# Kernel optimization log

Hardware: AMD Instinct MI355X
Metric: run time of the kernel (lower is better)

## Reference

```python
import jax, jax.numpy as jnp
import numpy as np

B, Tu, Tm, Tz = 32, 128, 128, 32
V, H, E = 10000, 512, 128
S = E + H  # state_size


def setup_inputs() -> dict:
    key = jax.random.key(0)
    ks = jax.random.split(key, 24)
    u_input = jax.random.randint(ks[0], (B, Tu), 0, V)
    m_input = jax.random.randint(ks[1], (B, Tm), 0, V)
    pv_z_idx = jax.random.randint(ks[2], (B, Tz), 0, V)
    inp = {
        'u_input': u_input,
        'u_input_1hot': jax.nn.one_hot(u_input, V, dtype=jnp.float32),
        'u_hiddens': jax.random.normal(ks[3], (B, Tu, H), jnp.float32),
        'm_input': m_input,
        'm_input_1hot': jax.nn.one_hot(m_input, V, dtype=jnp.float32),
        'm_hiddens': jax.random.normal(ks[4], (B, Tm, H), jnp.float32),
        'pv_z_prob': jax.nn.softmax(jax.random.normal(ks[5], (B, Tz, V), jnp.float32), axis=-1),
        'pv_z_hidden': jax.random.normal(ks[6], (B, Tz, H), jnp.float32),
        'pv_z_idx': pv_z_idx,
        'emb_zt': jax.random.normal(ks[7], (B, 1, E), jnp.float32),
        'last_hidden': jax.random.normal(ks[8], (1, B, H), jnp.float32),
        # Attn params (concat attention: v . tanh(W [h; enc]))
        'W_attn': jax.random.normal(ks[9], (H, 2 * H), jnp.float32) * 0.02,
        'b_attn': jnp.zeros((H,), jnp.float32),
        'v_attn': jax.random.normal(ks[10], (H,), jnp.float32) * 0.05,
        # GRU params (torch gate order r,z,n)
        'W_ih': jax.random.normal(ks[11], (3 * H, S), jnp.float32) * 0.02,
        'W_hh': jax.random.normal(ks[12], (3 * H, H), jnp.float32) * 0.02,
        'b_ih': jnp.zeros((3 * H,), jnp.float32),
        'b_hh': jnp.zeros((3 * H,), jnp.float32),
        # generation / copy-score projections
        'W_gen': jax.random.normal(ks[13], (V, S), jnp.float32) * 0.02,
        'b_gen': jnp.zeros((V,), jnp.float32),
        'W_cpu': jax.random.normal(ks[14], (S, H), jnp.float32) * 0.02,
        'b_cpu': jnp.zeros((S,), jnp.float32),
        'W_cpm': jax.random.normal(ks[15], (S, H), jnp.float32) * 0.02,
        'b_cpm': jnp.zeros((S,), jnp.float32),
        'W_cppz': jax.random.normal(ks[16], (S, H), jnp.float32) * 0.02,
        'b_cppz': jnp.zeros((S,), jnp.float32),
    }
    return inp


def reference(u_input, u_input_1hot, u_hiddens, m_input, m_input_1hot, m_hiddens,
              pv_z_prob, pv_z_hidden, pv_z_idx, emb_zt, last_hidden,
              W_attn, b_attn, v_attn, W_ih, W_hh, b_ih, b_hh,
              W_gen, b_gen, W_cpu, b_cpu, W_cpm, b_cpm, W_cppz, b_cppz):
    Bv, Tuv, Vv = u_input_1hot.shape
    Tmv = m_hiddens.shape[1]
    t_input = emb_zt  # [B,1,E] (enable_selc_read=False)

    # ---- concat attention over [u; m; pv_z] hiddens ----
    enc = jnp.concatenate([u_hiddens, m_hiddens, pv_z_hidden], axis=1)  # [B,T,H]
    h0 = jnp.transpose(last_hidden, (1, 0, 2))  # [B,1,H]
    hid_rep = jnp.broadcast_to(h0, (Bv, enc.shape[1], h0.shape[2]))
    energy = jnp.tanh(jnp.einsum('bth,gh->btg', jnp.concatenate([hid_rep, enc], axis=2), W_attn) + b_attn)
    attn_w = jax.nn.softmax(jnp.einsum('bth,h->bt', energy, v_attn), axis=1)
    context = jnp.einsum('bt,bth->bh', attn_w, enc)[:, None, :]  # [B,1,H]

    # ---- single GRU step (torch gate order r,z,n) ----
    x = jnp.concatenate([t_input, context], axis=2)[:, 0, :]  # [B,E+H]
    h = h0[:, 0, :]
    gi = x @ W_ih.T + b_ih
    gh = h @ W_hh.T + b_hh
    i_r, i_z, i_n = jnp.split(gi, 3, axis=1)
    h_r, h_z, h_n = jnp.split(gh, 3, axis=1)
    r = jax.nn.sigmoid(i_r + h_r)
    z = jax.nn.sigmoid(i_z + h_z)
    n = jnp.tanh(i_n + r * h_n)
    h_new = (1.0 - z) * n + z * h  # [B,H]
    gru_out = h_new[:, None, :]
    last_hidden_new = h_new[None, :, :]

    # ---- generation + copy scores ----
    st = jnp.concatenate([h_new, t_input[:, 0, :]], axis=1)  # [B,E+H]
    score_g = st @ W_gen.T + b_gen  # [B,V]
    sc_u = jnp.einsum('bts,bs->bt', jnp.tanh(jnp.einsum('bth,sh->bts', u_hiddens, W_cpu) + b_cpu), st)
    sc_m = jnp.einsum('bts,bs->bt', jnp.tanh(jnp.einsum('bth,sh->bts', m_hiddens, W_cpm) + b_cpm), st)
    sc_pz = jnp.einsum('bts,bs->bt', jnp.tanh(jnp.einsum('bth,sh->bts', pv_z_hidden, W_cppz) + b_cppz), st)
    probs = jax.nn.softmax(jnp.concatenate([score_g, sc_u, sc_m, sc_pz], axis=1), axis=1)

    p_g = probs[:, :Vv]
    p_u = probs[:, Vv:Vv + Tuv]
    p_m = probs[:, Vv + Tuv:Vv + Tuv + Tmv]
    p_pz = probs[:, Vv + Tuv + Tmv:]
    prob_out = (p_g
                + jnp.einsum('bt,btv->bv', p_u, u_input_1hot)
                + jnp.einsum('bt,btv->bv', p_m, m_input_1hot)
                + jnp.einsum('bt,btv->bv', p_pz, pv_z_prob))
    return (prob_out, last_hidden_new, gru_out)
```

## Files before the change

### kernel.cpp

```cpp
#include <hip/hip_runtime.h>
#include <math.h>

#define B   32
#define TU  128
#define TM  128
#define TZ  32
#define TENC 288
#define V   10000
#define H   512
#define E   128
#define S   640
#define G3  1536
#define NLOG (V + TENC)

#define WS_Q      0
#define WS_SCORE  (WS_Q + B*H)
#define WS_CTX    (WS_SCORE + B*TENC)
#define WS_GI     (WS_CTX + B*H)
#define WS_GH     (WS_GI + B*G3)
#define WS_ST     (WS_GH + B*G3)
#define WS_LOGIT  (WS_ST + B*S)
#define WS_PCOPY  (WS_LOGIT + B*NLOG)
#define WS_F_TOTAL (WS_PCOPY + B*TENC)

#define BF_WA2  0
#define BF_WCP  (BF_WA2 + 512*512)
#define BF_ENC  (BF_WCP + 3*640*512)
#define BF_ST   (BF_ENC + B*TENC*H)
#define BF_TANH (BF_ST + B*S)

typedef __attribute__((ext_vector_type(8))) short bf16x8_t;
typedef __attribute__((ext_vector_type(4))) float f32x4_t;
typedef __attribute__((ext_vector_type(16))) float f32x16_t;

__device__ __forceinline__ float fast_tanh(float x) {
    return 1.f - 2.f / (__expf(2.f * x) + 1.f);
}

__device__ __forceinline__ unsigned short f2bf(float x) {
    unsigned int u = __float_as_uint(x);
    u += 0x7fffu + ((u >> 16) & 1u);
    return (unsigned short)(u >> 16);
}

__device__ __forceinline__ float bf2f(unsigned short u) {
    return __uint_as_float(((unsigned int)u) << 16);
}

__device__ __forceinline__ bf16x8_t cvt8(const float* p) {
    float4 a = *(const float4*)(p);
    float4 b = *(const float4*)(p + 4);
    bf16x8_t r;
    r[0] = (short)f2bf(a.x); r[1] = (short)f2bf(a.y);
    r[2] = (short)f2bf(a.z); r[3] = (short)f2bf(a.w);
    r[4] = (short)f2bf(b.x); r[5] = (short)f2bf(b.y);
    r[6] = (short)f2bf(b.z); r[7] = (short)f2bf(b.w);
    return r;
}

__device__ __forceinline__ const float* enc_row(const float* u, const float* m,
                                                const float* pz, int b, int t) {
    if (t < TU) return u + ((size_t)b * TU + t) * H;
    if (t < TU + TM) return m + ((size_t)b * TM + (t - TU)) * H;
    return pz + ((size_t)b * TZ + (t - TU - TM)) * H;
}

#define CVT_WA2_END  65536
#define CVT_TOTAL    (CVT_WA2_END + 3*81920)
#define CVTE_TOTAL   (B * TENC * 128)
#define CVT_ALL      (CVT_TOTAL + CVTE_TOTAL)
#define NMV          112
__global__ __launch_bounds__(256) void k_prep(const float* __restrict__ W_attn,
                                              const float* __restrict__ W_cpu,
                                              const float* __restrict__ W_cpm,
                                              const float* __restrict__ W_cppz,
                                              const float* __restrict__ u_h,
                                              const float* __restrict__ m_h,
                                              const float* __restrict__ pz_h,
                                              const float* __restrict__ last_h,
                                              const float* __restrict__ emb,
                                              const float* __restrict__ W_hh,
                                              const float* __restrict__ W_ih,
                                              const float* __restrict__ b_attn,
                                              const float* __restrict__ b_hh,
                                              const float* __restrict__ b_ih,
                                              float* __restrict__ ws,
                                              unsigned short* __restrict__ bf) {
    int blk = blockIdx.x, tid = threadIdx.x;
    __shared__ float redmv[4][64][16];
    if (blk < NMV) {
        int wave = tid >> 6, lane = tid & 63;
        int m = lane & 31, khalf = lane >> 5;
        f32x16_t acc = {};
        int n;
        if (blk < 16) {
            n = blk * 32 + m;
            const float* aptr = last_h + (size_t)m * H + khalf * 8;
            const float* bptr = W_attn + (size_t)n * 1024 + khalf * 8;
            for (int k0 = wave * 128; k0 < wave * 128 + 128; k0 += 16)
                acc = __builtin_amdgcn_mfma_f32_32x32x16_bf16(cvt8(aptr + k0),
                                                              cvt8(bptr + k0), acc, 0, 0, 0);
        } else if (blk < 64) {
            n = (blk - 16) * 32 + m;
            const float* aptr = last_h + (size_t)m * H + khalf * 8;
            const float* bptr = W_hh + (size_t)n * H + khalf * 8;
            for (int k0 = wave * 128; k0 < wave * 128 + 128; k0 += 16)
                acc = __builtin_amdgcn_mfma_f32_32x32x16_bf16(cvt8(aptr + k0),
                                                              cvt8(bptr + k0), acc, 0, 0, 0);
        } else {
            n = (blk - 64) * 32 + m;
            const float* aptr = emb + (size_t)m * E + khalf * 8;
            const float* bptr = W_ih + (size_t)n * S + khalf * 8;
            for (int k0 = wave * 32; k0 < wave * 32 + 32; k0 += 16)
                acc = __builtin_amdgcn_mfma_f32_32x32x16_bf16(cvt8(aptr + k0),
                                                              cvt8(bptr + k0), acc, 0, 0, 0);
        }
#pragma unroll
        for (int r = 0; r < 16; ++r) redmv[wave][lane][r] = acc[r];
        __syncthreads();
        if (wave == 0) {
#pragma unroll
            for (int r = 0; r < 16; ++r) {
                float v = redmv[0][lane][r] + redmv[1][lane][r] +
                          redmv[2][lane][r] + redmv[3][lane][r];
                int row = (r & 3) + 8 * (r >> 2) + 4 * khalf;
                if (blk < 16)      ws[WS_Q  + row * H  + n] = v + b_attn[n];
                else if (blk < 64) ws[WS_GH + row * G3 + n] = v + b_hh[n];
                else               ws[WS_GI + row * G3 + n] = v + b_ih[n];
            }
        }
        return;
    }
    int idx = (blk - NMV) * 256 + tid;
    if (idx >= CVT_ALL) return;
    const float* src;
    unsigned short* dst;
    if (idx < CVT_WA2_END) {
        int g = idx >> 7, c4 = idx & 127;
        int k = c4 * 4, kt = k >> 5, kin = k & 31;
        src = W_attn + (size_t)g * 1024 + 512 + k;
        dst = bf + BF_WA2 + kt * (512 * 32) + g * 32 + kin;
    } else if (idx < CVT_TOTAL) {
        int r = idx - CVT_WA2_END;
        int seg = r / 81920, q = r % 81920;
        int s = q >> 7, c4 = q & 127;
        int k = c4 * 4, kt = k >> 5, kin = k & 31;
        const float* s0 = (seg == 0) ? W_cpu : (seg == 1) ? W_cpm : W_cppz;
        src = s0 + (size_t)s * 512 + k;
        dst = bf + BF_WCP + seg * 327680 + kt * (640 * 32) + s * 32 + kin;
    } else {
        int e = idx - CVT_TOTAL;
        int b = e / (TENC * 128);
        int r = e % (TENC * 128);
        int t = r >> 7, c4 = r & 127;
        int k = c4 * 4, kt = k >> 5, kin = k & 31;
        src = enc_row(u_h, m_h, pz_h, b, t) + k;
        dst = bf + BF_ENC + (((size_t)b * 16 + kt) * TENC + t) * 32 + kin;
    }
    float4 v = *(const float4*)src;
    ushort4 o;
    o.x = f2bf(v.x); o.y = f2bf(v.y); o.z = f2bf(v.z); o.w = f2bf(v.w);
    *(ushort4*)dst = o;
}

__global__ __launch_bounds__(256) void k_enc_mfma(const unsigned short* __restrict__ bf,
                                                  const float* __restrict__ v_attn,
                                                  const float* __restrict__ b_cpu,
                                                  const float* __restrict__ b_cpm,
                                                  const float* __restrict__ b_cppz,
                                                  float* __restrict__ ws,
                                                  unsigned short* __restrict__ bft) {
    int blk = blockIdx.x;
    int typeC = blk & 1;
    int idx = blk >> 1;
    int b = idx / 9, t0 = (idx % 9) * 32;
    int tid = threadIdx.x, wave = tid >> 6, lane = tid & 63;
    int n16 = lane & 15, quad = lane >> 4;
    const unsigned short* abase =
        bf + BF_ENC + (((size_t)b * 16) * TENC + t0 + n16) * 32 + quad * 8;
    if (!typeC) {
        const unsigned short* wa =
            bf + BF_WA2 + (wave * 8) * (16 * 32) + n16 * 32 + quad * 8;
        f32x4_t acc[2][8];
#pragma unroll
        for (int tl = 0; tl < 2; ++tl)
#pragma unroll
            for (int j = 0; j < 8; ++j) acc[tl][j] = (f32x4_t){0.f, 0.f, 0.f, 0.f};
        for (int kt = 0; kt < 16; ++kt) {
            bf16x8_t a0 = *(const bf16x8_t*)(abase + (size_t)kt * TENC * 32);
            bf16x8_t a1 = *(const bf16x8_t*)(abase + (size_t)kt * TENC * 32 + 16 * 32);
            const unsigned short* wak = wa + (size_t)kt * 512 * 32;
#pragma unroll
            for (int j = 0; j < 8; ++j) {
                bf16x8_t bb = *(const bf16x8_t*)(wak + j * (16 * 32));
                acc[0][j] = __builtin_amdgcn_mfma_f32_16x16x32_bf16(a0, bb, acc[0][j], 0, 0, 0);
                acc[1][j] = __builtin_amdgcn_mfma_f32_16x16x32_bf16(a1, bb, acc[1][j], 0, 0, 0);
            }
        }
        float sval[2][4] = {{0.f, 0.f, 0.f, 0.f}, {0.f, 0.f, 0.f, 0.f}};
#pragma unroll
        for (int j = 0; j < 8; ++j) {
            int g = (wave * 8 + j) * 16 + n16;
            float q = ws[WS_Q + b * H + g];
            float va = v_attn[g];
#pragma unroll
            for (int tl = 0; tl < 2; ++tl)
#pragma unroll
                for (int r = 0; r < 4; ++r)
                    sval[tl][r] += fast_tanh(acc[tl][j][r] + q) * va;
        }
#pragma unroll
        for (int tl = 0; tl < 2; ++tl)
#pragma unroll
            for (int r = 0; r < 4; ++r)
#pragma unroll
                for (int off = 8; off > 0; off >>= 1)
                    sval[tl][r] += __shfl_down(sval[tl][r], off, 64);
        __shared__ float red[4][32];
        if (n16 == 0)
#pragma unroll
            for (int tl = 0; tl < 2; ++tl)
#pragma unroll
                for (int r = 0; r < 4; ++r)
                    red[wave][tl * 16 + quad * 4 + r] = sval[tl][r];
        __syncthreads();
        if (tid < 32)
            ws[WS_SCORE + b * TENC + t0 + tid] =
                red[0][tid] + red[1][tid] + red[2][tid] + red[3][tid];
    } else {
        int seg = (t0 < TU) ? 0 : (t0 < TU + TM) ? 1 : 2;
        const float* bias = (seg == 0) ? b_cpu : (seg == 1) ? b_cpm : b_cppz;
        const unsigned short* wc =
            bf + BF_WCP + seg * 327680 + (wave * 10) * (16 * 32) + n16 * 32 + quad * 8;
        f32x4_t acc[2][10];
#pragma unroll
        for (int tl = 0; tl < 2; ++tl)
#pragma unroll
            for (int j = 0; j < 10; ++j) acc[tl][j] = (f32x4_t){0.f, 0.f, 0.f, 0.f};
        for (int kt = 0; kt < 16; ++kt) {
            bf16x8_t a0 = *(const bf16x8_t*)(abase + (size_t)kt * TENC * 32);
            bf16x8_t a1 = *(const bf16x8_t*)(abase + (size_t)kt * TENC * 32 + 16 * 32);
            const unsigned short* wck = wc + (size_t)kt * 640 * 32;
#pragma unroll
            for (int j = 0; j < 10; ++j) {
                bf16x8_t bb = *(const bf16x8_t*)(wck + j * (16 * 32));
                acc[0][j] = __builtin_amdgcn_mfma_f32_16x16x32_bf16(a0, bb, acc[0][j], 0, 0, 0);
                acc[1][j] = __builtin_amdgcn_mfma_f32_16x16x32_bf16(a1, bb, acc[1][j], 0, 0, 0);
            }
        }
#pragma unroll
        for (int j = 0; j < 10; ++j) {
            int s = (wave * 10 + j) * 16 + n16;
            float bi = bias[s];
#pragma unroll
            for (int tl = 0; tl < 2; ++tl)
#pragma unroll
                for (int r = 0; r < 4; ++r) {
                    int t = t0 + tl * 16 + quad * 4 + r;
                    bft[BF_TANH + ((size_t)b * TENC + t) * S + s] =
                        f2bf(fast_tanh(acc[tl][j][r] + bi));
                }
        }
    }
}

__global__ __launch_bounds__(256) void k_softmax_ctx(const unsigned short* __restrict__ bf,
                                                     float* __restrict__ ws) {
    int b = blockIdx.x, tid = threadIdx.x;
    __shared__ float wsm[TENC];
    __shared__ float red1[4], red2[4];
    float local = -1e30f;
    for (int t = tid; t < TENC; t += 256) {
        float s = ws[WS_SCORE + b * TENC + t];
        wsm[t] = s;
        local = fmaxf(local, s);
    }
    int lane = tid & 63, wv = tid >> 6;
    for (int off = 32; off > 0; off >>= 1) local = fmaxf(local, __shfl_down(local, off, 64));
    if (lane == 0) red1[wv] = local;
    __syncthreads();
    float mx = fmaxf(fmaxf(red1[0], red1[1]), fmaxf(red1[2], red1[3]));
    float ls = 0.f;
    for (int t = tid; t < TENC; t += 256) {
        float e = __expf(wsm[t] - mx);
        wsm[t] = e;
        ls += e;
    }
    for (int off = 32; off > 0; off >>= 1) ls += __shfl_down(ls, off, 64);
    if (lane == 0) red2[wv] = ls;
    __syncthreads();
    float inv = 1.f / (red2[0] + red2[1] + red2[2] + red2[3]);

    int h2 = tid * 2;
    int kt = h2 >> 5, hin = h2 & 31;
    const unsigned short* ep = bf + BF_ENC + ((size_t)b * 16 + kt) * TENC * 32 + hin;
    float a00 = 0.f, a01 = 0.f, a10 = 0.f, a11 = 0.f;
#pragma unroll 2
    for (int t = 0; t < TENC; t += 2) {
        ushort2 v0 = *(const ushort2*)(ep + (size_t)t * 32);
        ushort2 v1 = *(const ushort2*)(ep + (size_t)(t + 1) * 32);
        float w0 = wsm[t], w1 = wsm[t + 1];
        a00 += w0 * bf2f(v0.x); a10 += w0 * bf2f(v0.y);
        a01 += w1 * bf2f(v1.x); a11 += w1 * bf2f(v1.y);
    }
    ws[WS_CTX + b * H + h2]     = (a00 + a01) * inv;
    ws[WS_CTX + b * H + h2 + 1] = (a10 + a11) * inv;
}

__global__ __launch_bounds__(256) void k_gru_ctx(const float* __restrict__ W_ih,
                                                 float* __restrict__ ws) {
    int blk = blockIdx.x, tid = threadIdx.x;
    __shared__ float redmv[4][64][16];
    int wave = tid >> 6, lane = tid & 63;
    int m = lane & 31, khalf = lane >> 5;
    int n = blk * 32 + m;
    const float* aptr = ws + WS_CTX + (size_t)m * H + khalf * 8;
    const float* bptr = W_ih + (size_t)n * S + E + khalf * 8;
    f32x16_t acc = {};
    for (int k0 = wave * 128; k0 < wave * 128 + 128; k0 += 16)
        acc = __builtin_amdgcn_mfma_f32_32x32x16_bf16(cvt8(aptr + k0),
                                                      cvt8(bptr + k0), acc, 0, 0, 0);
#pragma unroll
    for (int r = 0; r < 16; ++r) redmv[wave][lane][r] = acc[r];
    __syncthreads();
    if (wave == 0) {
#pragma unroll
        for (int r = 0; r < 16; ++r) {
            float v = redmv[0][lane][r] + redmv[1][lane][r] +
                      redmv[2][lane][r] + redmv[3][lane][r];
            int row = (r & 3) + 8 * (r >> 2) + 4 * khalf;
            ws[WS_GI + row * G3 + n] += v;
        }
    }
}

__global__ __launch_bounds__(256) void k_combine(const float* __restrict__ emb,
                                                 const float* __restrict__ last_hidden,
                                                 float* __restrict__ ws,
                                                 unsigned short* __restrict__ bf,
                                                 float* __restrict__ out) {
    int i = blockIdx.x * 256 + threadIdx.x;
    int b = i >> 9, h = i & 511;
    float gi_r = ws[WS_GI + b * G3 + h];
    float gi_z = ws[WS_GI + b * G3 + H + h];
    float gi_n = ws[WS_GI + b * G3 + 2 * H + h];
    float gh_r = ws[WS_GH + b * G3 + h];
    float gh_z = ws[WS_GH + b * G3 + H + h];
    float gh_n = ws[WS_GH + b * G3 + 2 * H + h];
    float rr = 1.f / (1.f + __expf(-(gi_r + gh_r)));
    float zz = 1.f / (1.f + __expf(-(gi_z + gh_z)));
    float nn = fast_tanh(gi_n + rr * gh_n);
    float hp = last_hidden[b * H + h];
    float hn = (1.f - zz) * nn + zz * hp;
    out[V * B + b * H + h] = hn;
    out[V * B + B * H + b * H + h] = hn;
    ws[WS_ST + b * S + h] = hn;
    bf[BF_ST + b * S + h] = f2bf(hn);
    if (h < E) {
        float ev = emb[b * E + h];
        ws[WS_ST + b * S + H + h] = ev;
        bf[BF_ST + b * S + H + h] = f2bf(ev);
    }
}

__global__ __launch_bounds__(256) void k_logits(const unsigned short* __restrict__ bf,
                                                const float* __restrict__ W_gen,
                                                const float* __restrict__ b_gen,
                                                float* __restrict__ ws) {
    int blk = blockIdx.x, tid = threadIdx.x;
    __shared__ float shmem[4 * 64 * 16];
    int wave = tid >> 6, lane = tid & 63;
    if (blk < 576) {
        int b = blk / 18, t0 = (blk % 18) * 16;
        float* st_s = shmem;
        for (int i = tid; i < S; i += 256) st_s[i] = ws[WS_ST + b * S + i];
        __syncthreads();
#pragma unroll
        for (int tl = 0; tl < 4; ++tl) {
            int t = t0 + wave * 4 + tl;
            const unsigned short* row = bf + BF_TANH + ((size_t)b * TENC + t) * S;
            float acc = 0.f;
#pragma unroll
            for (int i = 0; i < 10; ++i) {
                int s = lane + 64 * i;
                acc += bf2f(row[s]) * st_s[s];
            }
            for (int off = 32; off > 0; off >>= 1) acc += __shfl_down(acc, off, 64);
            if (lane == 0) ws[WS_LOGIT + (size_t)b * NLOG + V + t] = acc;
        }
    } else {
        float (*redmv)[64][16] = (float (*)[64][16])shmem;
        int m = lane & 31, khalf = lane >> 5;
        int n = (blk - 576) * 32 + m;
        int nr = (n < V) ? n : (V - 1);
        const unsigned short* aptr = bf + BF_ST + (size_t)m * S + khalf * 8;
        const float* bptr = W_gen + (size_t)nr * S + khalf * 8;
        f32x16_t acc = {};
        for (int k0 = wave * 160; k0 < wave * 160 + 160; k0 += 16)
            acc = __builtin_amdgcn_mfma_f32_32x32x16_bf16(*(const bf16x8_t*)(aptr + k0),
                                                          cvt8(bptr + k0), acc, 0, 0, 0);
#pragma unroll
        for (int r = 0; r < 16; ++r) redmv[wave][lane][r] = acc[r];
        __syncthreads();
        if (wave == 0 && n < V) {
            float bg = b_gen[n];
#pragma unroll
            for (int r = 0; r < 16; ++r) {
                float v = redmv[0][lane][r] + redmv[1][lane][r] +
                          redmv[2][lane][r] + redmv[3][lane][r];
                int row = (r & 3) + 8 * (r >> 2) + 4 * khalf;
                ws[WS_LOGIT + (size_t)row * NLOG + n] = v + bg;
            }
        }
    }
}

__global__ __launch_bounds__(512) void k_softmax_scatter(const int* __restrict__ u_in,
                                                         const int* __restrict__ m_in,
                                                         float* __restrict__ ws,
                                                         float* __restrict__ out) {
    int b = blockIdx.x, tid = threadIdx.x;
    __shared__ float red1[8], red2[8];
    __shared__ float ex[NLOG];
    const float* lg = ws + WS_LOGIT + (size_t)b * NLOG;
    float mx = -1e30f;
    for (int i = tid; i < NLOG; i += 512) {
        float v = lg[i];
        ex[i] = v;
        mx = fmaxf(mx, v);
    }
    int lane = tid & 63, wv = tid >> 6;
    for (int off = 32; off > 0; off >>= 1) mx = fmaxf(mx, __shfl_down(mx, off, 64));
    if (lane == 0) red1[wv] = mx;
    __syncthreads();
    mx = red1[0];
#pragma unroll
    for (int w = 1; w < 8; ++w) mx = fmaxf(mx, red1[w]);
    float sm = 0.f;
    for (int i = tid; i < NLOG; i += 512) {
        float e = __expf(ex[i] - mx);
        ex[i] = e;
        sm += e;
    }
    for (int off = 32; off > 0; off >>= 1) sm += __shfl_down(sm, off, 64);
    if (lane == 0) red2[wv] = sm;
    __syncthreads();
    sm = red2[0];
#pragma unroll
    for (int w = 1; w < 8; ++w) sm += red2[w];
    float inv = 1.f / sm;
    for (int i = tid; i < V; i += 512) out[b * V + i] = ex[i] * inv;
    __syncthreads();
    if (tid < TU + TM) {
        int idx = (tid < TU) ? u_in[b * TU + tid] : m_in[b * TM + (tid - TU)];
        atomicAdd(&out[(size_t)b * V + idx], ex[V + tid] * inv);
    } else if (tid < TENC) {
        ws[WS_PCOPY + b * TENC + tid] = ex[V + tid] * inv;
    }
}

__global__ __launch_bounds__(256) void k_pv(const float* __restrict__ pvp,
                                            const float* __restrict__ ws,
                                            float* __restrict__ out) {
    int b = blockIdx.y;
    int v = blockIdx.x * 256 + threadIdx.x;
    __shared__ float p[TZ];
    if (threadIdx.x < TZ) p[threadIdx.x] = ws[WS_PCOPY + b * TENC + TU + TM + threadIdx.x];
    __syncthreads();
    if (v >= V) return;
    float acc = 0.f;
#pragma unroll 4
    for (int t = 0; t < TZ; ++t) acc += p[t] * pvp[((size_t)b * TZ + t) * V + v];
    out[(size_t)b * V + v] += acc;
}

extern "C" void kernel_launch(void* const* d_in, const int* in_sizes, int n_in,
                              void* d_out, int out_size, void* d_ws, size_t ws_size,
                              hipStream_t stream) {
    const int*   u_input   = (const int*)d_in[0];
    const float* u_h       = (const float*)d_in[2];
    const int*   m_input   = (const int*)d_in[3];
    const float* m_h       = (const float*)d_in[5];
    const float* pv_prob   = (const float*)d_in[6];
    const float* pz_h      = (const float*)d_in[7];
    const float* emb       = (const float*)d_in[9];
    const float* last_h    = (const float*)d_in[10];
    const float* W_attn    = (const float*)d_in[11];
    const float* b_attn    = (const float*)d_in[12];
    const float* v_attn    = (const float*)d_in[13];
    const float* W_ih      = (const float*)d_in[14];
    const float* W_hh      = (const float*)d_in[15];
    const float* b_ih      = (const float*)d_in[16];
    const float* b_hh      = (const float*)d_in[17];
    const float* W_gen     = (const float*)d_in[18];
    const float* b_gen     = (const float*)d_in[19];
    const float* W_cpu     = (const float*)d_in[20];
    const float* b_cpu     = (const float*)d_in[21];
    const float* W_cpm     = (const float*)d_in[22];
    const float* b_cpm     = (const float*)d_in[23];
    const float* W_cppz    = (const float*)d_in[24];
    const float* b_cppz    = (const float*)d_in[25];
    float* ws  = (float*)d_ws;
    unsigned short* bf = (unsigned short*)(ws + WS_F_TOTAL);
    float* out = (float*)d_out;

    hipLaunchKernelGGL(k_prep, dim3(NMV + CVT_ALL / 256), dim3(256), 0, stream,
                       W_attn, W_cpu, W_cpm, W_cppz, u_h, m_h, pz_h,
                       last_h, emb, W_hh, W_ih, b_attn, b_hh, b_ih, ws, bf);
    hipLaunchKernelGGL(k_enc_mfma, dim3(576), dim3(256), 0, stream,
                       bf, v_attn, b_cpu, b_cpm, b_cppz, ws, bf);
    hipLaunchKernelGGL(k_softmax_ctx, dim3(B), dim3(256), 0, stream, bf, ws);
    hipLaunchKernelGGL(k_gru_ctx, dim3(48), dim3(256), 0, stream, W_ih, ws);
    hipLaunchKernelGGL(k_combine, dim3(64), dim3(256), 0, stream, emb, last_h, ws, bf, out);
    hipLaunchKernelGGL(k_logits, dim3(576 + 313), dim3(256), 0, stream, bf, W_gen, b_gen, ws);
    hipLaunchKernelGGL(k_softmax_scatter, dim3(B), dim3(512), 0, stream,
                       u_input, m_input, ws, out);
    hipLaunchKernelGGL(k_pv, dim3(40, B), dim3(256), 0, stream, pv_prob, ws, out);
}
```

Measured before the change: 513.1 us.

## Stage encoder-MFMA weight and activation tiles through LDS per K-step

The encoder MFMA kernel now cooperatively copies each K-slice of the weight matrix and the 32-row activation tile into shared memory, with barriers around each step. Waves then read their MFMA fragments from LDS instead of issuing scattered global loads. Block assignment also changes from interleaving the two block types to running all attention-score blocks first and copy-score blocks after. This aims for coalesced global loads, but it adds two barriers per K-step, has no double buffering, and uses about 42KB of LDS per block, which may limit occupancy.

```diff
diff --git a/kernel.cpp b/kernel.cpp
--- a/kernel.cpp
+++ b/kernel.cpp
@@ -170,32 +170,46 @@
                                                   const float* __restrict__ b_cppz,
                                                   float* __restrict__ ws,
                                                   unsigned short* __restrict__ bft) {
+    __shared__ __attribute__((aligned(16))) unsigned short lds_w[640 * 32];
+    __shared__ __attribute__((aligned(16))) unsigned short lds_a[32 * 32];
+    __shared__ float red[4][32];
     int blk = blockIdx.x;
-    int typeC = blk & 1;
-    int idx = blk >> 1;
+    int typeC = (blk >= 288);
+    int idx = typeC ? blk - 288 : blk;
     int b = idx / 9, t0 = (idx % 9) * 32;
     int tid = threadIdx.x, wave = tid >> 6, lane = tid & 63;
     int n16 = lane & 15, quad = lane >> 4;
-    const unsigned short* abase =
-        bf + BF_ENC + (((size_t)b * 16) * TENC + t0 + n16) * 32 + quad * 8;
+    const unsigned short* asrc0 =
+        bf + BF_ENC + (((size_t)b * 16) * TENC + t0) * 32;
     if (!typeC) {
-        const unsigned short* wa =
-            bf + BF_WA2 + (wave * 8) * (16 * 32) + n16 * 32 + quad * 8;
         f32x4_t acc[2][8];
 #pragma unroll
         for (int tl = 0; tl < 2; ++tl)
 #pragma unroll
             for (int j = 0; j < 8; ++j) acc[tl][j] = (f32x4_t){0.f, 0.f, 0.f, 0.f};
         for (int kt = 0; kt < 16; ++kt) {
-            bf16x8_t a0 = *(const bf16x8_t*)(abase + (size_t)kt * TENC * 32);
-            bf16x8_t a1 = *(const bf16x8_t*)(abase + (size_t)kt * TENC * 32 + 16 * 32);
-            const unsigned short* wak = wa + (size_t)kt * 512 * 32;
+            const unsigned short* wsrc = bf + BF_WA2 + (size_t)kt * (512 * 32);
+#pragma unroll
+            for (int c = 0; c < 8; ++c) {
+                int u = (c * 256 + tid) * 8;
+                *(bf16x8_t*)&lds_w[u] = *(const bf16x8_t*)&wsrc[u];
+            }
+            if (tid < 128) {
+                int u = tid * 8;
+                *(bf16x8_t*)&lds_a[u] =
+                    *(const bf16x8_t*)&asrc0[(size_t)kt * TENC * 32 + u];
+            }
+            __syncthreads();
+            bf16x8_t a0 = *(const bf16x8_t*)&lds_a[n16 * 32 + quad * 8];
+            bf16x8_t a1 = *(const bf16x8_t*)&lds_a[(n16 + 16) * 32 + quad * 8];
 #pragma unroll
             for (int j = 0; j < 8; ++j) {
-                bf16x8_t bb = *(const bf16x8_t*)(wak + j * (16 * 32));
+                bf16x8_t bb = *(const bf16x8_t*)
+                    &lds_w[((wave * 8 + j) * 16 + n16) * 32 + quad * 8];
                 acc[0][j] = __builtin_amdgcn_mfma_f32_16x16x32_bf16(a0, bb, acc[0][j], 0, 0, 0);
                 acc[1][j] = __builtin_amdgcn_mfma_f32_16x16x32_bf16(a1, bb, acc[1][j], 0, 0, 0);
             }
+            __syncthreads();
         }
         float sval[2][4] = {{0.f, 0.f, 0.f, 0.f}, {0.f, 0.f, 0.f, 0.f}};
 #pragma unroll
@@ -216,7 +230,6 @@
 #pragma unroll
                 for (int off = 8; off > 0; off >>= 1)
                     sval[tl][r] += __shfl_down(sval[tl][r], off, 64);
-        __shared__ float red[4][32];
         if (n16 == 0)
 #pragma unroll
             for (int tl = 0; tl < 2; ++tl)
@@ -230,23 +243,35 @@
     } else {
         int seg = (t0 < TU) ? 0 : (t0 < TU + TM) ? 1 : 2;
         const float* bias = (seg == 0) ? b_cpu : (seg == 1) ? b_cpm : b_cppz;
-        const unsigned short* wc =
-            bf + BF_WCP + seg * 327680 + (wave * 10) * (16 * 32) + n16 * 32 + quad * 8;
         f32x4_t acc[2][10];
 #pragma unroll
         for (int tl = 0; tl < 2; ++tl)
 #pragma unroll
             for (int j = 0; j < 10; ++j) acc[tl][j] = (f32x4_t){0.f, 0.f, 0.f, 0.f};
         for (int kt = 0; kt < 16; ++kt) {
-            bf16x8_t a0 = *(const bf16x8_t*)(abase + (size_t)kt * TENC * 32);
-            bf16x8_t a1 = *(const bf16x8_t*)(abase + (size_t)kt * TENC * 32 + 16 * 32);
-            const unsigned short* wck = wc + (size_t)kt * 640 * 32;
+            const unsigned short* wsrc =
+                bf + BF_WCP + seg * 327680 + (size_t)kt * (640 * 32);
+#pragma unroll
+            for (int c = 0; c < 10; ++c) {
+                int u = (c * 256 + tid) * 8;
+                *(bf16x8_t*)&lds_w[u] = *(const bf16x8_t*)&wsrc[u];
+            }
+            if (tid < 128) {
+                int u = tid * 8;
+                *(bf16x8_t*)&lds_a[u] =
+                    *(const bf16x8_t*)&asrc0[(size_t)kt * TENC * 32 + u];
+            }
+            __syncthreads();
+            bf16x8_t a0 = *(const bf16x8_t*)&lds_a[n16 * 32 + quad * 8];
+            bf16x8_t a1 = *(const bf16x8_t*)&lds_a[(n16 + 16) * 32 + quad * 8];
 #pragma unroll
             for (int j = 0; j < 10; ++j) {
-                bf16x8_t bb = *(const bf16x8_t*)(wck + j * (16 * 32));
+                bf16x8_t bb = *(const bf16x8_t*)
+                    &lds_w[((wave * 10 + j) * 16 + n16) * 32 + quad * 8];
                 acc[0][j] = __builtin_amdgcn_mfma_f32_16x16x32_bf16(a0, bb, acc[0][j], 0, 0, 0);
                 acc[1][j] = __builtin_amdgcn_mfma_f32_16x16x32_bf16(a1, bb, acc[1][j], 0, 0, 0);
             }
+            __syncthreads();
         }
 #pragma unroll
         for (int j = 0; j < 10; ++j) {
```

Result: faster. 468.1 us (-8.8%).
